# Performance work log

Measured on AMD Instinct MI355X. Metric: run time of the kernel, lower is better.

The kernel has to match this reference:

```python
import jax, jax.numpy as jnp
import numpy as np

POT_BETA = 0.5
ONS_MIN_D = 0.1
DT = 0.01
B, N, H = 65536, 32, 128  # batch, nVar (n_dim), hidden width


def f_act(x):
    r = jax.nn.relu(x)
    r2 = jax.nn.relu(x - 0.5)
    return r * r - r2 * r2


def setup_inputs() -> dict:
    key = jax.random.key(0)
    ks = jax.random.split(key, 14)

    def xav(k, shape, gain=0.1):
        fan_out, fan_in = shape
        lim = gain * np.sqrt(6.0 / (fan_in + fan_out))
        return jax.random.uniform(k, shape, jnp.float32, -lim, lim)

    def ubias(k, shape, hi=0.05):
        return jax.random.uniform(k, shape, jnp.float32, 0.0, hi)

    return {
        "z0": jax.random.normal(ks[0], (B, N), jnp.float32),
        "noise": jax.random.normal(ks[1], (B, N), jnp.float32),
        "W0": xav(ks[2], (H, N)),      # baselayer[0]
        "b0": ubias(ks[3], (H,)),
        "W1": xav(ks[4], (H, H)),      # baselayer[1] (ResNet)
        "b1": ubias(ks[5], (H,)),
        "Wm": xav(ks[6], (N * N, H)),  # MatLayer
        "bm": jax.random.normal(ks[7], (N * N,), jnp.float32) * 0.1,
        "Wp": xav(ks[8], (N, H)),      # PotLayer
        "bp": ubias(ks[9], (N,), 0.1),
        "Wpl": xav(ks[10], (N, N)),    # PotLinear
        "bpl": ubias(ks[11], (N,), 0.1),
        "sigma_kernel": jnp.ones((N,), jnp.float32),  # constant_diagonal DiffusitivityNet
    }


def reference(z0, noise, W0, b0, W1, b1, Wm, bm, Wp, bp, Wpl, bpl, sigma_kernel):
    n = z0.shape[-1]

    def hidden(x):
        h = f_act(x @ W0.T + b0)
        h = f_act(h @ W1.T + b1) + h  # ResNet skip on layer 1
        return h

    def pot_scalar(xi):  # xi: [n] -> scalar potential V for one sample
        h = hidden(xi)
        pot = h @ Wp.T + bp + xi @ Wpl.T + bpl
        return jnp.sum(pot * pot) + POT_BETA * jnp.sum(xi * xi)

    # g = -dV/dx, per sample (torch.autograd.grad of summed V == per-sample grads)
    g = -jax.vmap(jax.grad(pot_scalar))(z0)  # [B, n]

    h = hidden(z0)  # [B, H]
    matA = (h @ Wm.T + bm).reshape(-1, n, n)  # [B, n, n]
    AL = jnp.tril(matA)
    AU = jnp.triu(matA, 1)
    # MW = antisymmetric(AU) + PSD(AL @ AL^T)
    MW = (AU - jnp.swapaxes(AU, 1, 2)) + jnp.einsum('bik,bjk->bij', AL, AL)
    drift = jnp.einsum('bij,bj->bi', MW, g) + ONS_MIN_D * g  # [B, n]

    # constant_diagonal sigma: einsum('ijk,ik->ij', diag(kernel), noise) == kernel * noise
    z1 = z0 + drift * DT + (noise * sigma_kernel) * jnp.sqrt(jnp.float32(DT))
    return z1
```

## Files before the change

### kernel.cpp

```cpp
#include <hip/hip_runtime.h>
#include <stdint.h>

typedef unsigned int u32;
typedef unsigned short u16;
typedef __attribute__((ext_vector_type(8))) short bf16x8;
typedef __attribute__((ext_vector_type(4))) float f32x4;

#define N_DIM 32
#define H_DIM 128
#define SPW 4
#define SBLK 16
#define AB_RS 34
#define AB_SS 1090

#define CW2    0
#define CW0F   16384
#define CW1F   16896
#define CW1T   18944
#define CWPF   20992
#define CWPT   21504
#define CWPLF  22016
#define CWPLT  22144
#define CW0T   22272
#define CEND   22784

__device__ __forceinline__ float bflo(u32 u) { return __uint_as_float(u << 16); }
__device__ __forceinline__ float bfhi(u32 u) { return __uint_as_float(u & 0xffff0000u); }
__device__ __forceinline__ float bf1(u16 u) { return __uint_as_float(((u32)u) << 16); }
__device__ __forceinline__ u16 f2bf(float f) {
    u32 u = __float_as_uint(f);
    u += 0x7fffu + ((u >> 16) & 1u);
    return (u16)(u >> 16);
}
__device__ __forceinline__ float factf(float x) {
    float r = fmaxf(x, 0.f), r2 = fmaxf(x - 0.5f, 0.f);
    return r * r - r2 * r2;
}
__device__ __forceinline__ float dact(float x) {
    return 2.f * fminf(fmaxf(x, 0.f), 0.5f);
}

template<bool BF> __device__ __forceinline__ float ld1(const void* p, int i) {
    if constexpr (BF) return __uint_as_float(((u32)(((const u16*)p)[i])) << 16);
    else              return ((const float*)p)[i];
}
template<bool BF> __device__ __forceinline__ float2 ld2(const void* p, int i) {
    if constexpr (BF) { u32 u = *(const u32*)((const u16*)p + i); return make_float2(bflo(u), bfhi(u)); }
    else              { return *(const float2*)((const float*)p + i); }
}
template<bool BF> __device__ __forceinline__ void st2(void* p, int i, float a, float b) {
    if constexpr (BF) { u32 o = (u32)f2bf(a) | ((u32)f2bf(b) << 16); *(u32*)((u16*)p + i) = o; }
    else              { *(float2*)((float*)p + i) = make_float2(a, b); }
}

__global__ __launch_bounds__(256) void repack_all(
    const void* W0, const void* W1, const void* Wm,
    const void* Wp, const void* Wpl, const void* sig, u16* W)
{
    const int c = blockIdx.x * 256 + threadIdx.x;
    if (c >= CEND) return;
    const bool bf = (*(const u32*)sig) != 0x3F800000u;
    const void* src; int LD, local, KS; bool T;
    if      (c < CW0F)  { src = Wm;  LD = 128; T = false; local = c - CW2;   KS = 4; }
    else if (c < CW1F)  { src = W0;  LD = 32;  T = false; local = c - CW0F;  KS = 1; }
    else if (c < CW1T)  { src = W1;  LD = 128; T = false; local = c - CW1F;  KS = 4; }
    else if (c < CWPF)  { src = W1;  LD = 128; T = true;  local = c - CW1T;  KS = 4; }
    else if (c < CWPT)  { src = Wp;  LD = 128; T = false; local = c - CWPF;  KS = 4; }
    else if (c < CWPLF) { src = Wp;  LD = 128; T = true;  local = c - CWPT;  KS = 1; }
    else if (c < CWPLT) { src = Wpl; LD = 32;  T = false; local = c - CWPLF; KS = 1; }
    else if (c < CW0T)  { src = Wpl; LD = 32;  T = true;  local = c - CWPLT; KS = 1; }
    else                { src = W0;  LD = 32;  T = true;  local = c - CW0T;  KS = 4; }
    const int ln = local & 63;
    const int ks = (local >> 6) & (KS - 1);
    const int nt = local / (KS * 64);
    const int k  = ks * 32 + (ln >> 4) * 8;
    const int n  = nt * 16 + (ln & 15);
    u16 o[8];
#pragma unroll
    for (int e = 0; e < 8; ++e) {
        const int kk = k + e;
        const int si = T ? (kk * LD + n) : (n * LD + kk);
        o[e] = bf ? ((const u16*)src)[si] : f2bf(((const float*)src)[si]);
    }
    u32* dst = (u32*)(W + (size_t)c * 8);
    dst[0] = (u32)o[0] | ((u32)o[1] << 16);
    dst[1] = (u32)o[2] | ((u32)o[3] << 16);
    dst[2] = (u32)o[4] | ((u32)o[5] << 16);
    dst[3] = (u32)o[6] | ((u32)o[7] << 16);
}

#define MFMA16(a, b, c) __builtin_amdgcn_mfma_f32_16x16x32_bf16((a), (b), (c), 0, 0, 0)

template<bool BF>
__device__ __forceinline__ void body(
    const void* z0, const void* noise, const void* b0, const void* b1,
    const void* bm, const void* bp, const void* bpl, const void* sig,
    const bf16x8* WS, void* out, int Btot,
    u16* Ab2, u16* h2a, u16* h2b, float* xb, u16* x2, u16* u2, float* gbuf)
{
    const int t = threadIdx.x;
    const int w = t >> 6, l = t & 63;
    const int cn = l & 15, lh = l >> 4;
    const int pidx = blockIdx.x * 256 + t;
    const int npair = Btot * (N_DIM / 2);

    {
        float2 xz = (pidx < npair) ? ld2<BF>(z0, 2 * pidx) : make_float2(0.f, 0.f);
        xb[2 * t] = xz.x; xb[2 * t + 1] = xz.y;
        const int s = t >> 4, j0 = 2 * (t & 15);
        *(u32*)&x2[((j0 >> 3) * 16 + s) * 8 + (j0 & 7)] =
            (u32)f2bf(xz.x) | ((u32)f2bf(xz.y) << 16);
    }
    __syncthreads();

    const bf16x8 afx = *(const bf16x8*)&x2[(lh * 16 + cn) * 8];

    float h0r[2][4], d0r[2][4], d1r[2][4], ghr[2][4];

#pragma unroll
    for (int t2 = 0; t2 < 2; ++t2) {
        const int nt = 2 * w + t2, n = nt * 16 + cn;
        f32x4 acc = {0.f, 0.f, 0.f, 0.f};
        acc = MFMA16(afx, WS[CW0F + nt * 64 + l], acc);
        const float b0v = ld1<BF>(b0, n);
#pragma unroll
        for (int r = 0; r < 4; ++r) {
            const float a0 = acc[r] + b0v;
            h0r[t2][r] = factf(a0); d0r[t2][r] = dact(a0);
            h2a[((n >> 3) * 16 + (lh * 4 + r)) * 8 + (n & 7)] = f2bf(h0r[t2][r]);
        }
    }
    __syncthreads();

    {
        bf16x8 afh[4];
#pragma unroll
        for (int ks = 0; ks < 4; ++ks)
            afh[ks] = *(const bf16x8*)&h2a[((ks * 4 + lh) * 16 + cn) * 8];
#pragma unroll
        for (int t2 = 0; t2 < 2; ++t2) {
            const int nt = 2 * w + t2, n = nt * 16 + cn;
            f32x4 acc = {0.f, 0.f, 0.f, 0.f};
#pragma unroll
            for (int ks = 0; ks < 4; ++ks)
                acc = MFMA16(afh[ks], WS[CW1F + (nt * 4 + ks) * 64 + l], acc);
            const float b1v = ld1<BF>(b1, n);
#pragma unroll
            for (int r = 0; r < 4; ++r) {
                const float a1 = acc[r] + b1v;
                d1r[t2][r] = dact(a1);
                h2b[((n >> 3) * 16 + (lh * 4 + r)) * 8 + (n & 7)] =
                    f2bf(factf(a1) + h0r[t2][r]);
            }
        }
    }
    __syncthreads();

    if (w < 2) {
        const int nt = w, n = nt * 16 + cn;
        f32x4 acc = {0.f, 0.f, 0.f, 0.f};
#pragma unroll
        for (int ks = 0; ks < 4; ++ks) {
            const bf16x8 af = *(const bf16x8*)&h2b[((ks * 4 + lh) * 16 + cn) * 8];
            acc = MFMA16(af, WS[CWPF + (nt * 4 + ks) * 64 + l], acc);
        }
        acc = MFMA16(afx, WS[CWPLF + nt * 64 + l], acc);
        const float pb = ld1<BF>(bp, n) + ld1<BF>(bpl, n);
#pragma unroll
        for (int r = 0; r < 4; ++r) {
            const float uv = 2.f * (acc[r] + pb);
            u2[((n >> 3) * 16 + (lh * 4 + r)) * 8 + (n & 7)] = f2bf(uv);
        }
    }
    __syncthreads();

    const bf16x8 afu = *(const bf16x8*)&u2[(lh * 16 + cn) * 8];

#pragma unroll
    for (int t2 = 0; t2 < 2; ++t2) {
        const int nt = 2 * w + t2, n = nt * 16 + cn;
        f32x4 acc = {0.f, 0.f, 0.f, 0.f};
        acc = MFMA16(afu, WS[CWPT + nt * 64 + l], acc);
#pragma unroll
        for (int r = 0; r < 4; ++r) {
            ghr[t2][r] = acc[r];
            h2a[((n >> 3) * 16 + (lh * 4 + r)) * 8 + (n & 7)] = f2bf(acc[r] * d1r[t2][r]);
        }
    }
    __syncthreads();

    {
        bf16x8 afg[4];
#pragma unroll
        for (int ks = 0; ks < 4; ++ks)
            afg[ks] = *(const bf16x8*)&h2a[((ks * 4 + lh) * 16 + cn) * 8];
#pragma unroll
        for (int t2 = 0; t2 < 2; ++t2) {
            const int nt = 2 * w + t2, n = nt * 16 + cn;
            f32x4 acc = {0.f, 0.f, 0.f, 0.f};
#pragma unroll
            for (int ks = 0; ks < 4; ++ks)
                acc = MFMA16(afg[ks], WS[CW1T + (nt * 4 + ks) * 64 + l], acc);
#pragma unroll
            for (int r = 0; r < 4; ++r) {
                const float ga0v = (acc[r] + ghr[t2][r]) * d0r[t2][r];
                Ab2[((n >> 3) * 16 + (lh * 4 + r)) * 8 + (n & 7)] = f2bf(ga0v);
            }
        }
    }
    __syncthreads();

    if (w < 2) {
        const int nt = w, n = nt * 16 + cn;
        f32x4 acc = {0.f, 0.f, 0.f, 0.f};
#pragma unroll
        for (int ks = 0; ks < 4; ++ks) {
            const bf16x8 af = *(const bf16x8*)&Ab2[((ks * 4 + lh) * 16 + cn) * 8];
            acc = MFMA16(af, WS[CW0T + (nt * 4 + ks) * 64 + l], acc);
        }
        acc = MFMA16(afu, WS[CWPLT + nt * 64 + l], acc);
#pragma unroll
        for (int r = 0; r < 4; ++r) {
            const int s = lh * 4 + r;
            gbuf[s * N_DIM + n] = -(xb[s * N_DIM + n] + acc[r]);
        }
    }
    __syncthreads();

    {
        const bf16x8 af0 = *(const bf16x8*)&h2b[((0 * 4 + lh) * 16 + cn) * 8];
        const bf16x8 af1 = *(const bf16x8*)&h2b[((1 * 4 + lh) * 16 + cn) * 8];
        const bf16x8 af2 = *(const bf16x8*)&h2b[((2 * 4 + lh) * 16 + cn) * 8];
        const bf16x8 af3 = *(const bf16x8*)&h2b[((3 * 4 + lh) * 16 + cn) * 8];
#pragma unroll 2
        for (int nt = 0; nt < 16; ++nt) {
            const int cb = (w * 16 + nt) * 256 + l;
            const bf16x8 bv0 = WS[cb];
            const bf16x8 bv1 = WS[cb + 64];
            const bf16x8 bv2 = WS[cb + 128];
            const bf16x8 bv3 = WS[cb + 192];
            f32x4 acc = {0.f, 0.f, 0.f, 0.f};
            acc = MFMA16(af0, bv0, acc);
            acc = MFMA16(af1, bv1, acc);
            acc = MFMA16(af2, bv2, acc);
            acc = MFMA16(af3, bv3, acc);
            const int m = w * 256 + nt * 16 + cn;
            const int i = m >> 5, j = m & 31;
            const int sg = lh * 4;
            Ab2[(sg + 0) * AB_SS + i * AB_RS + j] = f2bf(acc[0]);
            Ab2[(sg + 1) * AB_SS + i * AB_RS + j] = f2bf(acc[1]);
            Ab2[(sg + 2) * AB_SS + i * AB_RS + j] = f2bf(acc[2]);
            Ab2[(sg + 3) * AB_SS + i * AB_RS + j] = f2bf(acc[3]);
        }
    }
    __syncthreads();

    float* ubuf = (float*)h2b;
    float* dbuf = ubuf + 512;
    {
        const int c = l & 31, ih = l >> 5;
        float bmA[16], bmB[16];
#pragma unroll
        for (int r = 0; r < 16; ++r)  bmA[r]  = ld1<BF>(bm, (ih * 16 + r) * N_DIM + c);
#pragma unroll
        for (int c2 = 0; c2 < 16; ++c2) bmB[c2] = ld1<BF>(bm, c * N_DIM + ih * 16 + c2);
#pragma unroll
        for (int ss = 0; ss < SPW; ++ss) {
            const int s = w * SPW + ss;
            const u16* As = &Ab2[s * AB_SS];
            const float* gs = &gbuf[s * N_DIM];
            float yp = 0.f, tp = 0.f;
#pragma unroll
            for (int r = 0; r < 16; ++r) {
                const int i = ih * 16 + r;
                const float a = bf1(As[i * AB_RS + c]) + bmA[r];
                const float gi = gs[i];
                if (i >= c) yp = fmaf(a, gi, yp); else tp = fmaf(a, gi, tp);
            }
            const float yv = yp + __shfl_xor(yp, 32);
            const float tv = tp + __shfl_xor(tp, 32);
            if (l < 32) { ubuf[s * N_DIM + c] = yv; dbuf[s * N_DIM + c] = -tv; }
            float au = 0.f;
#pragma unroll
            for (int c2 = 0; c2 < 16; ++c2) {
                const int j = ih * 16 + c2;
                const float a = bf1(As[c * AB_RS + j]) + bmB[c2];
                const float gj = (j > c)  ? gs[j] : 0.f;
                const float yj = (j <= c) ? ubuf[s * N_DIM + j] : 0.f;
                au = fmaf(a, gj, au);
                au = fmaf(a, yj, au);
            }
            au += __shfl_xor(au, 32);
            if (l < 32) dbuf[s * N_DIM + c] += au;
        }
    }

    if (pidx < npair) {
        const float2 nz2 = ld2<BF>(noise, 2 * pidx);
        const int e0 = 2 * t;
        const int jj = e0 & 31;
        const float sg0 = ld1<BF>(sig, jj), sg1 = ld1<BF>(sig, jj + 1);
        const float dr0 = dbuf[e0]     + 0.1f * gbuf[e0];
        const float dr1 = dbuf[e0 + 1] + 0.1f * gbuf[e0 + 1];
        const float z10 = xb[e0]     + dr0 * 0.01f + nz2.x * sg0 * 0.1f;
        const float z11 = xb[e0 + 1] + dr1 * 0.01f + nz2.y * sg1 * 0.1f;
        st2<BF>(out, 2 * pidx, z10, z11);
    }
}

__global__ __launch_bounds__(256, 3) void onsager_step(
    const void* z0, const void* noise, const void* b0, const void* b1,
    const void* bm, const void* bp, const void* bpl, const void* sig,
    const void* ws, void* out, int Btot)
{
    __shared__ __align__(16) u16   Ab2[SBLK * AB_SS];
    __shared__ __align__(16) u16   h2a[2048];
    __shared__ __align__(16) u16   h2b[2048];
    __shared__ __align__(16) float xb[SBLK * N_DIM];
    __shared__ __align__(16) u16   x2[512];
    __shared__ __align__(16) u16   u2[512];
    __shared__ __align__(16) float gbuf[SBLK * N_DIM];

    const u32 sigbits = *(const u32*)sig;
    if (sigbits == 0x3F800000u)
        body<false>(z0, noise, b0, b1, bm, bp, bpl, sig, (const bf16x8*)ws, out, Btot,
                    Ab2, h2a, h2b, xb, x2, u2, gbuf);
    else
        body<true >(z0, noise, b0, b1, bm, bp, bpl, sig, (const bf16x8*)ws, out, Btot,
                    Ab2, h2a, h2b, xb, x2, u2, gbuf);
}

extern "C" void kernel_launch(void* const* d_in, const int* in_sizes, int n_in,
                              void* d_out, int out_size, void* d_ws, size_t ws_size,
                              hipStream_t stream) {
    const void* z0  = d_in[0];
    const void* nz  = d_in[1];
    const void* W0  = d_in[2];
    const void* b0  = d_in[3];
    const void* W1  = d_in[4];
    const void* b1  = d_in[5];
    const void* Wm  = d_in[6];
    const void* bm  = d_in[7];
    const void* Wp  = d_in[8];
    const void* bp  = d_in[9];
    const void* Wpl = d_in[10];
    const void* bpl = d_in[11];
    const void* sig = d_in[12];

    const int Btot = in_sizes[0] / N_DIM;
    u16* W = (u16*)d_ws;

    repack_all<<<dim3(89), dim3(256), 0, stream>>>(W0, W1, Wm, Wp, Wpl, sig, W);

    dim3 grid((Btot + SBLK - 1) / SBLK), block(256);
    onsager_step<<<grid, block, 0, stream>>>(z0, nz, b0, b1, bm, bp, bpl, sig,
                                             d_ws, d_out, Btot);
}
```

Measured before the change: 173.7 us.

## Double samples per block and reuse weight fragments across two sample tiles

Raises the block to 512 threads handling 32 samples, so each wave loads its weight MFMA fragments once and applies them to two 16-sample tiles. The MatLayer GEMM is reoriented so weights are the A operand, and the bias is folded in with packed bf16 conversion. Other changes: the gradient's x term is added through an identity-matrix MFMA, g is stored as bf16, z0 stays in registers, and shared buffers are aliased to cut LDS use. In exchange, g loses precision by being stored in bf16, register pressure is higher, and the block count is halved.

```diff
diff --git a/kernel.cpp b/kernel.cpp
--- a/kernel.cpp
+++ b/kernel.cpp
@@ -9,7 +9,8 @@
 #define N_DIM 32
 #define H_DIM 128
 #define SPW 4
-#define SBLK 16
+#define SBLK 32
+#define NTHR 512
 #define AB_RS 34
 #define AB_SS 1090
 
@@ -22,7 +23,8 @@
 #define CWPLF  22016
 #define CWPLT  22144
 #define CW0T   22272
-#define CEND   22784
+#define CIDT   22784
+#define CEND   22912
 
 __device__ __forceinline__ float bflo(u32 u) { return __uint_as_float(u << 16); }
 __device__ __forceinline__ float bfhi(u32 u) { return __uint_as_float(u & 0xffff0000u); }
@@ -32,6 +34,11 @@
     u += 0x7fffu + ((u >> 16) & 1u);
     return (u16)(u >> 16);
 }
+__device__ __forceinline__ u32 cvtpk(float a, float b) {
+    u32 r;
+    asm("v_cvt_pk_bf16_f32 %0, %1, %2" : "=v"(r) : "v"(a), "v"(b));
+    return r;
+}
 __device__ __forceinline__ float factf(float x) {
     float r = fmaxf(x, 0.f), r2 = fmaxf(x - 0.5f, 0.f);
     return r * r - r2 * r2;
@@ -47,6 +54,11 @@
 template<bool BF> __device__ __forceinline__ float2 ld2(const void* p, int i) {
     if constexpr (BF) { u32 u = *(const u32*)((const u16*)p + i); return make_float2(bflo(u), bfhi(u)); }
     else              { return *(const float2*)((const float*)p + i); }
+}
+template<bool BF> __device__ __forceinline__ float4 ld4(const void* p, int i) {
+    if constexpr (BF) { uint2 u = *(const uint2*)((const u16*)p + i);
+        return make_float4(bflo(u.x), bfhi(u.x), bflo(u.y), bfhi(u.y)); }
+    else              { return *(const float4*)((const float*)p + i); }
 }
 template<bool BF> __device__ __forceinline__ void st2(void* p, int i, float a, float b) {
     if constexpr (BF) { u32 o = (u32)f2bf(a) | ((u32)f2bf(b) << 16); *(u32*)((u16*)p + i) = o; }
@@ -60,27 +72,34 @@
     const int c = blockIdx.x * 256 + threadIdx.x;
     if (c >= CEND) return;
     const bool bf = (*(const u32*)sig) != 0x3F800000u;
-    const void* src; int LD, local, KS; bool T;
-    if      (c < CW0F)  { src = Wm;  LD = 128; T = false; local = c - CW2;   KS = 4; }
-    else if (c < CW1F)  { src = W0;  LD = 32;  T = false; local = c - CW0F;  KS = 1; }
-    else if (c < CW1T)  { src = W1;  LD = 128; T = false; local = c - CW1F;  KS = 4; }
-    else if (c < CWPF)  { src = W1;  LD = 128; T = true;  local = c - CW1T;  KS = 4; }
-    else if (c < CWPT)  { src = Wp;  LD = 128; T = false; local = c - CWPF;  KS = 4; }
-    else if (c < CWPLF) { src = Wp;  LD = 128; T = true;  local = c - CWPT;  KS = 1; }
-    else if (c < CWPLT) { src = Wpl; LD = 32;  T = false; local = c - CWPLF; KS = 1; }
-    else if (c < CW0T)  { src = Wpl; LD = 32;  T = true;  local = c - CWPLT; KS = 1; }
-    else                { src = W0;  LD = 32;  T = true;  local = c - CW0T;  KS = 4; }
-    const int ln = local & 63;
-    const int ks = (local >> 6) & (KS - 1);
-    const int nt = local / (KS * 64);
-    const int k  = ks * 32 + (ln >> 4) * 8;
-    const int n  = nt * 16 + (ln & 15);
     u16 o[8];
-#pragma unroll
-    for (int e = 0; e < 8; ++e) {
-        const int kk = k + e;
-        const int si = T ? (kk * LD + n) : (n * LD + kk);
-        o[e] = bf ? ((const u16*)src)[si] : f2bf(((const float*)src)[si]);
+    if (c >= CIDT) {
+        const int local = c - CIDT, ln = local & 63, nt = local >> 6;
+        const int k = (ln >> 4) * 8, n = nt * 16 + (ln & 15);
+#pragma unroll
+        for (int e = 0; e < 8; ++e) o[e] = (k + e == n) ? (u16)0x3F80 : (u16)0;
+    } else {
+        const void* src; int LD, local, KS; bool T;
+        if      (c < CW0F)  { src = Wm;  LD = 128; T = false; local = c - CW2;   KS = 4; }
+        else if (c < CW1F)  { src = W0;  LD = 32;  T = false; local = c - CW0F;  KS = 1; }
+        else if (c < CW1T)  { src = W1;  LD = 128; T = false; local = c - CW1F;  KS = 4; }
+        else if (c < CWPF)  { src = W1;  LD = 128; T = true;  local = c - CW1T;  KS = 4; }
+        else if (c < CWPT)  { src = Wp;  LD = 128; T = false; local = c - CWPF;  KS = 4; }
+        else if (c < CWPLF) { src = Wp;  LD = 128; T = true;  local = c - CWPT;  KS = 1; }
+        else if (c < CWPLT) { src = Wpl; LD = 32;  T = false; local = c - CWPLF; KS = 1; }
+        else if (c < CW0T)  { src = Wpl; LD = 32;  T = true;  local = c - CWPLT; KS = 1; }
+        else                { src = W0;  LD = 32;  T = true;  local = c - CW0T;  KS = 4; }
+        const int ln = local & 63;
+        const int ks = (local >> 6) & (KS - 1);
+        const int nt = local / (KS * 64);
+        const int k  = ks * 32 + (ln >> 4) * 8;
+        const int n  = nt * 16 + (ln & 15);
+#pragma unroll
+        for (int e = 0; e < 8; ++e) {
+            const int kk = k + e;
+            const int si = T ? (kk * LD + n) : (n * LD + kk);
+            o[e] = bf ? ((const u16*)src)[si] : f2bf(((const float*)src)[si]);
+        }
     }
     u32* dst = (u32*)(W + (size_t)c * 8);
     dst[0] = (u32)o[0] | ((u32)o[1] << 16);
@@ -96,185 +115,205 @@
     const void* z0, const void* noise, const void* b0, const void* b1,
     const void* bm, const void* bp, const void* bpl, const void* sig,
     const bf16x8* WS, void* out, int Btot,
-    u16* Ab2, u16* h2a, u16* h2b, float* xb, u16* x2, u16* u2, float* gbuf)
+    u16* Ab2, u16* h2b, u16* g2)
 {
     const int t = threadIdx.x;
     const int w = t >> 6, l = t & 63;
     const int cn = l & 15, lh = l >> 4;
-    const int pidx = blockIdx.x * 256 + t;
+    const int pidx = blockIdx.x * NTHR + t;
     const int npair = Btot * (N_DIM / 2);
 
-    {
-        float2 xz = (pidx < npair) ? ld2<BF>(z0, 2 * pidx) : make_float2(0.f, 0.f);
-        xb[2 * t] = xz.x; xb[2 * t + 1] = xz.y;
+    u16* h2a = Ab2;
+    u16* gaf = Ab2 + 4096;
+    u16* x2  = Ab2 + 8192;
+    u16* u2  = Ab2 + 9216;
+
+    const float2 xz = (pidx < npair) ? ld2<BF>(z0, 2 * pidx) : make_float2(0.f, 0.f);
+    {
         const int s = t >> 4, j0 = 2 * (t & 15);
-        *(u32*)&x2[((j0 >> 3) * 16 + s) * 8 + (j0 & 7)] =
+        *(u32*)&x2[((j0 >> 3) * 32 + s) * 8 + (j0 & 7)] =
             (u32)f2bf(xz.x) | ((u32)f2bf(xz.y) << 16);
     }
     __syncthreads();
 
-    const bf16x8 afx = *(const bf16x8*)&x2[(lh * 16 + cn) * 8];
+    const bf16x8 afx0 = *(const bf16x8*)&x2[(lh * 32 + cn) * 8];
+    const bf16x8 afx1 = *(const bf16x8*)&x2[(lh * 32 + 16 + cn) * 8];
 
     float h0r[2][4], d0r[2][4], d1r[2][4], ghr[2][4];
 
-#pragma unroll
-    for (int t2 = 0; t2 < 2; ++t2) {
-        const int nt = 2 * w + t2, n = nt * 16 + cn;
-        f32x4 acc = {0.f, 0.f, 0.f, 0.f};
-        acc = MFMA16(afx, WS[CW0F + nt * 64 + l], acc);
-        const float b0v = ld1<BF>(b0, n);
-#pragma unroll
-        for (int r = 0; r < 4; ++r) {
-            const float a0 = acc[r] + b0v;
-            h0r[t2][r] = factf(a0); d0r[t2][r] = dact(a0);
-            h2a[((n >> 3) * 16 + (lh * 4 + r)) * 8 + (n & 7)] = f2bf(h0r[t2][r]);
-        }
-    }
-    __syncthreads();
-
-    {
-        bf16x8 afh[4];
-#pragma unroll
-        for (int ks = 0; ks < 4; ++ks)
-            afh[ks] = *(const bf16x8*)&h2a[((ks * 4 + lh) * 16 + cn) * 8];
-#pragma unroll
-        for (int t2 = 0; t2 < 2; ++t2) {
-            const int nt = 2 * w + t2, n = nt * 16 + cn;
+    {
+        const bf16x8 wb = WS[CW0F + w * 64 + l];
+        const float b0v = ld1<BF>(b0, w * 16 + cn);
+        const int n = w * 16 + cn;
+#pragma unroll
+        for (int st = 0; st < 2; ++st) {
             f32x4 acc = {0.f, 0.f, 0.f, 0.f};
-#pragma unroll
-            for (int ks = 0; ks < 4; ++ks)
-                acc = MFMA16(afh[ks], WS[CW1F + (nt * 4 + ks) * 64 + l], acc);
-            const float b1v = ld1<BF>(b1, n);
+            acc = MFMA16(st ? afx1 : afx0, wb, acc);
+#pragma unroll
+            for (int r = 0; r < 4; ++r) {
+                const float a0 = acc[r] + b0v;
+                h0r[st][r] = factf(a0); d0r[st][r] = dact(a0);
+                const int s = st * 16 + lh * 4 + r;
+                h2a[((n >> 3) * 32 + s) * 8 + (n & 7)] = f2bf(h0r[st][r]);
+            }
+        }
+    }
+    __syncthreads();
+
+    {
+        const float b1v = ld1<BF>(b1, w * 16 + cn);
+        const int n = w * 16 + cn;
+        bf16x8 wb[4];
+#pragma unroll
+        for (int ks = 0; ks < 4; ++ks) wb[ks] = WS[CW1F + (w * 4 + ks) * 64 + l];
+#pragma unroll
+        for (int st = 0; st < 2; ++st) {
+            f32x4 acc = {0.f, 0.f, 0.f, 0.f};
+#pragma unroll
+            for (int ks = 0; ks < 4; ++ks) {
+                const bf16x8 af = *(const bf16x8*)&h2a[((ks * 4 + lh) * 32 + st * 16 + cn) * 8];
+                acc = MFMA16(af, wb[ks], acc);
+            }
 #pragma unroll
             for (int r = 0; r < 4; ++r) {
                 const float a1 = acc[r] + b1v;
-                d1r[t2][r] = dact(a1);
-                h2b[((n >> 3) * 16 + (lh * 4 + r)) * 8 + (n & 7)] =
-                    f2bf(factf(a1) + h0r[t2][r]);
-            }
-        }
-    }
-    __syncthreads();
-
-    if (w < 2) {
-        const int nt = w, n = nt * 16 + cn;
+                d1r[st][r] = dact(a1);
+                const int s = st * 16 + lh * 4 + r;
+                h2b[((n >> 3) * 32 + s) * 8 + (n & 7)] = f2bf(factf(a1) + h0r[st][r]);
+            }
+        }
+    }
+    __syncthreads();
+
+    if (w < 4) {
+        const int st = w >> 1, ntP = w & 1;
+        const int n = ntP * 16 + cn;
         f32x4 acc = {0.f, 0.f, 0.f, 0.f};
 #pragma unroll
         for (int ks = 0; ks < 4; ++ks) {
-            const bf16x8 af = *(const bf16x8*)&h2b[((ks * 4 + lh) * 16 + cn) * 8];
-            acc = MFMA16(af, WS[CWPF + (nt * 4 + ks) * 64 + l], acc);
-        }
-        acc = MFMA16(afx, WS[CWPLF + nt * 64 + l], acc);
+            const bf16x8 af = *(const bf16x8*)&h2b[((ks * 4 + lh) * 32 + st * 16 + cn) * 8];
+            acc = MFMA16(af, WS[CWPF + (ntP * 4 + ks) * 64 + l], acc);
+        }
+        acc = MFMA16(st ? afx1 : afx0, WS[CWPLF + ntP * 64 + l], acc);
         const float pb = ld1<BF>(bp, n) + ld1<BF>(bpl, n);
 #pragma unroll
         for (int r = 0; r < 4; ++r) {
-            const float uv = 2.f * (acc[r] + pb);
-            u2[((n >> 3) * 16 + (lh * 4 + r)) * 8 + (n & 7)] = f2bf(uv);
-        }
-    }
-    __syncthreads();
-
-    const bf16x8 afu = *(const bf16x8*)&u2[(lh * 16 + cn) * 8];
-
-#pragma unroll
-    for (int t2 = 0; t2 < 2; ++t2) {
-        const int nt = 2 * w + t2, n = nt * 16 + cn;
+            const int s = st * 16 + lh * 4 + r;
+            u2[((n >> 3) * 32 + s) * 8 + (n & 7)] = f2bf(2.f * (acc[r] + pb));
+        }
+    }
+    __syncthreads();
+
+    const bf16x8 afu0 = *(const bf16x8*)&u2[(lh * 32 + cn) * 8];
+    const bf16x8 afu1 = *(const bf16x8*)&u2[(lh * 32 + 16 + cn) * 8];
+
+    {
+        const bf16x8 wb = WS[CWPT + w * 64 + l];
+        const int n = w * 16 + cn;
+#pragma unroll
+        for (int st = 0; st < 2; ++st) {
+            f32x4 acc = {0.f, 0.f, 0.f, 0.f};
+            acc = MFMA16(st ? afu1 : afu0, wb, acc);
+#pragma unroll
+            for (int r = 0; r < 4; ++r) {
+                ghr[st][r] = acc[r];
+                const int s = st * 16 + lh * 4 + r;
+                h2a[((n >> 3) * 32 + s) * 8 + (n & 7)] = f2bf(acc[r] * d1r[st][r]);
+            }
+        }
+    }
+    __syncthreads();
+
+    {
+        const int n = w * 16 + cn;
+        bf16x8 wb[4];
+#pragma unroll
+        for (int ks = 0; ks < 4; ++ks) wb[ks] = WS[CW1T + (w * 4 + ks) * 64 + l];
+#pragma unroll
+        for (int st = 0; st < 2; ++st) {
+            f32x4 acc = {0.f, 0.f, 0.f, 0.f};
+#pragma unroll
+            for (int ks = 0; ks < 4; ++ks) {
+                const bf16x8 af = *(const bf16x8*)&h2a[((ks * 4 + lh) * 32 + st * 16 + cn) * 8];
+                acc = MFMA16(af, wb[ks], acc);
+            }
+#pragma unroll
+            for (int r = 0; r < 4; ++r) {
+                const float ga0v = (acc[r] + ghr[st][r]) * d0r[st][r];
+                const int s = st * 16 + lh * 4 + r;
+                gaf[((n >> 3) * 32 + s) * 8 + (n & 7)] = f2bf(ga0v);
+            }
+        }
+    }
+    __syncthreads();
+
+    if (w < 4) {
+        const int st = w >> 1, ntP = w & 1;
+        const int n = ntP * 16 + cn;
         f32x4 acc = {0.f, 0.f, 0.f, 0.f};
-        acc = MFMA16(afu, WS[CWPT + nt * 64 + l], acc);
+#pragma unroll
+        for (int ks = 0; ks < 4; ++ks) {
+            const bf16x8 af = *(const bf16x8*)&gaf[((ks * 4 + lh) * 32 + st * 16 + cn) * 8];
+            acc = MFMA16(af, WS[CW0T + (ntP * 4 + ks) * 64 + l], acc);
+        }
+        acc = MFMA16(st ? afu1 : afu0, WS[CWPLT + ntP * 64 + l], acc);
+        acc = MFMA16(st ? afx1 : afx0, WS[CIDT + ntP * 64 + l], acc);
 #pragma unroll
         for (int r = 0; r < 4; ++r) {
-            ghr[t2][r] = acc[r];
-            h2a[((n >> 3) * 16 + (lh * 4 + r)) * 8 + (n & 7)] = f2bf(acc[r] * d1r[t2][r]);
-        }
-    }
-    __syncthreads();
-
-    {
-        bf16x8 afg[4];
-#pragma unroll
-        for (int ks = 0; ks < 4; ++ks)
-            afg[ks] = *(const bf16x8*)&h2a[((ks * 4 + lh) * 16 + cn) * 8];
-#pragma unroll
-        for (int t2 = 0; t2 < 2; ++t2) {
-            const int nt = 2 * w + t2, n = nt * 16 + cn;
-            f32x4 acc = {0.f, 0.f, 0.f, 0.f};
-#pragma unroll
-            for (int ks = 0; ks < 4; ++ks)
-                acc = MFMA16(afg[ks], WS[CW1T + (nt * 4 + ks) * 64 + l], acc);
-#pragma unroll
-            for (int r = 0; r < 4; ++r) {
-                const float ga0v = (acc[r] + ghr[t2][r]) * d0r[t2][r];
-                Ab2[((n >> 3) * 16 + (lh * 4 + r)) * 8 + (n & 7)] = f2bf(ga0v);
-            }
-        }
-    }
-    __syncthreads();
-
-    if (w < 2) {
-        const int nt = w, n = nt * 16 + cn;
-        f32x4 acc = {0.f, 0.f, 0.f, 0.f};
+            const int s = st * 16 + lh * 4 + r;
+            g2[s * N_DIM + n] = f2bf(-acc[r]);
+        }
+    }
+    __syncthreads();
+
+    {
+        bf16x8 bh0[4], bh1[4];
 #pragma unroll
         for (int ks = 0; ks < 4; ++ks) {
-            const bf16x8 af = *(const bf16x8*)&Ab2[((ks * 4 + lh) * 16 + cn) * 8];
-            acc = MFMA16(af, WS[CW0T + (nt * 4 + ks) * 64 + l], acc);
-        }
-        acc = MFMA16(afu, WS[CWPLT + nt * 64 + l], acc);
-#pragma unroll
-        for (int r = 0; r < 4; ++r) {
-            const int s = lh * 4 + r;
-            gbuf[s * N_DIM + n] = -(xb[s * N_DIM + n] + acc[r]);
-        }
-    }
-    __syncthreads();
-
-    {
-        const bf16x8 af0 = *(const bf16x8*)&h2b[((0 * 4 + lh) * 16 + cn) * 8];
-        const bf16x8 af1 = *(const bf16x8*)&h2b[((1 * 4 + lh) * 16 + cn) * 8];
-        const bf16x8 af2 = *(const bf16x8*)&h2b[((2 * 4 + lh) * 16 + cn) * 8];
-        const bf16x8 af3 = *(const bf16x8*)&h2b[((3 * 4 + lh) * 16 + cn) * 8];
+            bh0[ks] = *(const bf16x8*)&h2b[((ks * 4 + lh) * 32 + cn) * 8];
+            bh1[ks] = *(const bf16x8*)&h2b[((ks * 4 + lh) * 32 + 16 + cn) * 8];
+        }
 #pragma unroll 2
-        for (int nt = 0; nt < 16; ++nt) {
-            const int cb = (w * 16 + nt) * 256 + l;
-            const bf16x8 bv0 = WS[cb];
-            const bf16x8 bv1 = WS[cb + 64];
-            const bf16x8 bv2 = WS[cb + 128];
-            const bf16x8 bv3 = WS[cb + 192];
-            f32x4 acc = {0.f, 0.f, 0.f, 0.f};
-            acc = MFMA16(af0, bv0, acc);
-            acc = MFMA16(af1, bv1, acc);
-            acc = MFMA16(af2, bv2, acc);
-            acc = MFMA16(af3, bv3, acc);
-            const int m = w * 256 + nt * 16 + cn;
-            const int i = m >> 5, j = m & 31;
-            const int sg = lh * 4;
-            Ab2[(sg + 0) * AB_SS + i * AB_RS + j] = f2bf(acc[0]);
-            Ab2[(sg + 1) * AB_SS + i * AB_RS + j] = f2bf(acc[1]);
-            Ab2[(sg + 2) * AB_SS + i * AB_RS + j] = f2bf(acc[2]);
-            Ab2[(sg + 3) * AB_SS + i * AB_RS + j] = f2bf(acc[3]);
+        for (int mt = 0; mt < 8; ++mt) {
+            const int mtg = w * 8 + mt;
+            bf16x8 wa[4];
+#pragma unroll
+            for (int ks = 0; ks < 4; ++ks) wa[ks] = WS[CW2 + (mtg * 4 + ks) * 64 + l];
+            const int m0 = mtg * 16 + lh * 4;
+            const float4 bmv = ld4<BF>(bm, m0);
+            const int i  = mtg >> 1;
+            const int jb = (mtg & 1) * 16 + lh * 4;
+#pragma unroll
+            for (int st = 0; st < 2; ++st) {
+                f32x4 acc = {0.f, 0.f, 0.f, 0.f};
+                acc = MFMA16(wa[0], st ? bh1[0] : bh0[0], acc);
+                acc = MFMA16(wa[1], st ? bh1[1] : bh0[1], acc);
+                acc = MFMA16(wa[2], st ? bh1[2] : bh0[2], acc);
+                acc = MFMA16(wa[3], st ? bh1[3] : bh0[3], acc);
+                const int s = st * 16 + cn;
+                u32* dst = (u32*)&Ab2[s * AB_SS + i * AB_RS + jb];
+                dst[0] = cvtpk(acc[0] + bmv.x, acc[1] + bmv.y);
+                dst[1] = cvtpk(acc[2] + bmv.z, acc[3] + bmv.w);
+            }
         }
     }
     __syncthreads();
 
     float* ubuf = (float*)h2b;
-    float* dbuf = ubuf + 512;
+    float* dbuf = ubuf + SBLK * N_DIM;
     {
         const int c = l & 31, ih = l >> 5;
-        float bmA[16], bmB[16];
-#pragma unroll
-        for (int r = 0; r < 16; ++r)  bmA[r]  = ld1<BF>(bm, (ih * 16 + r) * N_DIM + c);
-#pragma unroll
-        for (int c2 = 0; c2 < 16; ++c2) bmB[c2] = ld1<BF>(bm, c * N_DIM + ih * 16 + c2);
 #pragma unroll
         for (int ss = 0; ss < SPW; ++ss) {
             const int s = w * SPW + ss;
             const u16* As = &Ab2[s * AB_SS];
-            const float* gs = &gbuf[s * N_DIM];
+            const u16* gs = &g2[s * N_DIM];
             float yp = 0.f, tp = 0.f;
 #pragma unroll
             for (int r = 0; r < 16; ++r) {
                 const int i = ih * 16 + r;
-                const float a = bf1(As[i * AB_RS + c]) + bmA[r];
-                const float gi = gs[i];
+                const float a = bf1(As[i * AB_RS + c]);
+                const float gi = bf1(gs[i]);
                 if (i >= c) yp = fmaf(a, gi, yp); else tp = fmaf(a, gi, tp);
             }
             const float yv = yp + __shfl_xor(yp, 32);
@@ -282,13 +321,15 @@
             if (l < 32) { ubuf[s * N_DIM + c] = yv; dbuf[s * N_DIM + c] = -tv; }
             float au = 0.f;
 #pragma unroll
-            for (int c2 = 0; c2 < 16; ++c2) {
-                const int j = ih * 16 + c2;
-                const float a = bf1(As[c * AB_RS + j]) + bmB[c2];
-                const float gj = (j > c)  ? gs[j] : 0.f;
-                const float yj = (j <= c) ? ubuf[s * N_DIM + j] : 0.f;
-                au = fmaf(a, gj, au);
-                au = fmaf(a, yj, au);
+            for (int q = 0; q < 8; ++q) {
+                const int j0 = ih * 16 + 2 * q;
+                const u32 av = *(const u32*)&As[c * AB_RS + j0];
+                const u32 gv = *(const u32*)&gs[j0];
+                const float2 yv2 = *(const float2*)&ubuf[s * N_DIM + j0];
+                const float s0 = (j0     > c) ? bflo(gv) : yv2.x;
+                const float s1 = (j0 + 1 > c) ? bfhi(gv) : yv2.y;
+                au = fmaf(bflo(av), s0, au);
+                au = fmaf(bfhi(av), s1, au);
             }
             au += __shfl_xor(au, 32);
             if (l < 32) dbuf[s * N_DIM + c] += au;
@@ -300,34 +341,31 @@
         const int e0 = 2 * t;
         const int jj = e0 & 31;
         const float sg0 = ld1<BF>(sig, jj), sg1 = ld1<BF>(sig, jj + 1);
-        const float dr0 = dbuf[e0]     + 0.1f * gbuf[e0];
-        const float dr1 = dbuf[e0 + 1] + 0.1f * gbuf[e0 + 1];
-        const float z10 = xb[e0]     + dr0 * 0.01f + nz2.x * sg0 * 0.1f;
-        const float z11 = xb[e0 + 1] + dr1 * 0.01f + nz2.y * sg1 * 0.1f;
+        const u32 gv = *(const u32*)&g2[e0];
+        const float dr0 = dbuf[e0]     + 0.1f * bflo(gv);
+        const float dr1 = dbuf[e0 + 1] + 0.1f * bfhi(gv);
+        const float z10 = xz.x + dr0 * 0.01f + nz2.x * sg0 * 0.1f;
+        const float z11 = xz.y + dr1 * 0.01f + nz2.y * sg1 * 0.1f;
         st2<BF>(out, 2 * pidx, z10, z11);
     }
 }
 
-__global__ __launch_bounds__(256, 3) void onsager_step(
+__global__ __launch_bounds__(512, 4) void onsager_step(
     const void* z0, const void* noise, const void* b0, const void* b1,
     const void* bm, const void* bp, const void* bpl, const void* sig,
     const void* ws, void* out, int Btot)
 {
-    __shared__ __align__(16) u16   Ab2[SBLK * AB_SS];
-    __shared__ __align__(16) u16   h2a[2048];
-    __shared__ __align__(16) u16   h2b[2048];
-    __shared__ __align__(16) float xb[SBLK * N_DIM];
-    __shared__ __align__(16) u16   x2[512];
-    __shared__ __align__(16) u16   u2[512];
-    __shared__ __align__(16) float gbuf[SBLK * N_DIM];
+    __shared__ __align__(16) u16 Ab2[SBLK * AB_SS];
+    __shared__ __align__(16) u16 h2b[SBLK * H_DIM];
+    __shared__ __align__(16) u16 g2 [SBLK * N_DIM];
 
     const u32 sigbits = *(const u32*)sig;
     if (sigbits == 0x3F800000u)
         body<false>(z0, noise, b0, b1, bm, bp, bpl, sig, (const bf16x8*)ws, out, Btot,
-                    Ab2, h2a, h2b, xb, x2, u2, gbuf);
+                    Ab2, h2b, g2);
     else
         body<true >(z0, noise, b0, b1, bm, bp, bpl, sig, (const bf16x8*)ws, out, Btot,
-                    Ab2, h2a, h2b, xb, x2, u2, gbuf);
+                    Ab2, h2b, g2);
 }
 
 extern "C" void kernel_launch(void* const* d_in, const int* in_sizes, int n_in,
@@ -350,9 +388,9 @@
     const int Btot = in_sizes[0] / N_DIM;
     u16* W = (u16*)d_ws;
 
-    repack_all<<<dim3(89), dim3(256), 0, stream>>>(W0, W1, Wm, Wp, Wpl, sig, W);
-
-    dim3 grid((Btot + SBLK - 1) / SBLK), block(256);
+    repack_all<<<dim3((CEND + 255) / 256), dim3(256), 0, stream>>>(W0, W1, Wm, Wp, Wpl, sig, W);
+
+    dim3 grid((Btot + SBLK - 1) / SBLK), block(NTHR);
     onsager_step<<<grid, block, 0, stream>>>(z0, nz, b0, b1, bm, bp, bpl, sig,
                                              d_ws, d_out, Btot);
 }
```

Measured after the change: 147.7 us. 1.18x faster.
